# Optimization experiments

Hardware: AMD Instinct MI355X
Metric: run time of the kernel (lower is better)

## Reference

```python
import jax, jax.numpy as jnp
import numpy as np

# irrep blocks for 0e+1o+2e: dims 1, 3, 5 (total D=9)
BLOCKS = [(0, 1), (1, 4), (4, 9)]

def block_linear(x, W):
    # x: [N, C, 9], W: [3, C, C] -- e3nn Linear mixes channels within each irrep block
    outs = [jnp.einsum('ncd,cq->nqd', x[..., s:e], W[l]) for l, (s, e) in enumerate(BLOCKS)]
    return jnp.concatenate(outs, axis=-1)

def setup_inputs() -> dict:
    key = jax.random.key(0)
    ks = jax.random.split(key, 14)
    N, E, C, D, B, H, Z = 16384, 262144, 32, 9, 8, 64, 4
    inp = {
        'node_feats': jax.random.normal(ks[0], (N, C, D), jnp.float32),
        'node_attrs': jax.random.uniform(ks[1], (N, Z), jnp.float32),
        'edge_feats': jax.random.normal(ks[2], (E, B), jnp.float32),
        'edge_sh': jax.random.normal(ks[3], (E, D), jnp.float32),
        'cutoff': jax.random.uniform(ks[4], (E, 1), jnp.float32),
        # learned params
        'W_up': jax.random.normal(ks[5], (3, C, C), jnp.float32) / np.float32(np.sqrt(C)),
        'W1': jax.random.normal(ks[6], (B, H), jnp.float32) / np.float32(np.sqrt(B)),
        'W2': jax.random.normal(ks[7], (H, H), jnp.float32) / np.float32(np.sqrt(H)),
        'W3': jax.random.normal(ks[8], (H, C), jnp.float32) / np.float32(np.sqrt(H)),
        'W_lin': jax.random.normal(ks[9], (3, C, C), jnp.float32) / np.float32(np.sqrt(C)),
        'W_sc': jax.random.normal(ks[10], (Z, 3, C, C), jnp.float32) / np.float32(np.sqrt(C)),
        # fixed Clebsch-Gordan-like coupling tensor (constant structure of the TP)
        'CG': jax.random.normal(ks[11], (D, D, D), jnp.float32) / np.float32(D),
        'edge_src': jax.random.randint(ks[12], (E,), 0, N, jnp.int32),
        'edge_dst': jax.random.randint(ks[13], (E,), 0, N, jnp.int32),
    }
    return inp

def reference(node_feats, node_attrs, edge_feats, edge_sh, cutoff,
              W_up, W1, W2, W3, W_lin, W_sc, CG, edge_src, edge_dst):
    N = node_feats.shape[0]
    avg_num_neighbors = 16.0
    # linear_up: per-irrep channel mixing
    x = block_linear(node_feats, W_up)
    # radial MLP -> per-edge tensor-product weights, gated by cutoff
    h = jax.nn.silu(edge_feats @ W1)
    h = jax.nn.silu(h @ W2)
    w = (h @ W3) * cutoff  # [E, C]
    # gather source node feats, weighted equivariant tensor product per edge
    xs = x[edge_src]  # [E, C, D]
    m_ij = jnp.einsum('eci,ej,ijk,ec->eck', xs, edge_sh, CG, w)  # [E, C, D]
    # scatter-sum aggregation into destination nodes
    m_i = jax.ops.segment_sum(m_ij, edge_dst, num_segments=N)  # [N, C, D]
    # output linear + neighbor normalization
    m_i = block_linear(m_i, W_lin) / avg_num_neighbors
    # element-dependent self-connection from current message
    W_node = jnp.einsum('nz,zlcq->nlcq', node_attrs, W_sc)  # [N, 3, C, C]
    scs = jnp.concatenate(
        [jnp.einsum('ncd,ncq->nqd', m_i[..., s:e], W_node[:, l]) for l, (s, e) in enumerate(BLOCKS)],
        axis=-1)
    return (m_i, scs)
```

## Files before the change

kernel.cpp:

```cpp
#include <hip/hip_runtime.h>
#include <cstdint>

#define CC 32
#define DD 9
#define CD 288
#define BB 8
#define HH 64
#define ZZ 4
#define NB 8

typedef __attribute__((ext_vector_type(8))) short bf16x8;
typedef __attribute__((ext_vector_type(4))) float f32x4;

__device__ __forceinline__ float silu_f(float v) {
  return v / (1.0f + __expf(-v));
}

__device__ __forceinline__ int blk_of(int d) { return d == 0 ? 0 : (d < 4 ? 1 : 2); }

__device__ __forceinline__ unsigned int f2bf(float f) {
  unsigned int u = __float_as_uint(f);
  return (u + 0x7fffu + ((u >> 16) & 1u)) >> 16;
}
__device__ __forceinline__ float bf_lo(unsigned int u) { return __uint_as_float(u << 16); }
__device__ __forceinline__ float bf_hi(unsigned int u) { return __uint_as_float(u & 0xffff0000u); }

__global__ __launch_bounds__(256) void k_zero(float* __restrict__ p, int n) {
  int i = blockIdx.x * 256 + threadIdx.x;
  if (i < n) p[i] = 0.0f;
}

__global__ __launch_bounds__(256) void k_hist(const int* __restrict__ edst,
                                              int* __restrict__ deg, int E) {
  int e = blockIdx.x * 256 + threadIdx.x;
  if (e < E) atomicAdd(&deg[edst[e]], 1);
}

__global__ __launch_bounds__(1024) void k_scan(const int* __restrict__ deg,
                                               int* __restrict__ offs,
                                               int* __restrict__ cursor, int N) {
  __shared__ int part[1024];
  int t = threadIdx.x;
  int chunk = (N + 1023) >> 10;
  int base = t * chunk;
  int lim = N - base; if (lim > chunk) lim = chunk; if (lim < 0) lim = 0;
  int s = 0;
  for (int i = 0; i < lim; ++i) s += deg[base + i];
  part[t] = s;
  __syncthreads();
  for (int off = 1; off < 1024; off <<= 1) {
    int v = part[t];
    int u = (t >= off) ? part[t - off] : 0;
    __syncthreads();
    part[t] = v + u;
    __syncthreads();
  }
  int run = (t == 0) ? 0 : part[t - 1];
  for (int i = 0; i < lim; ++i) {
    offs[base + i] = run;
    cursor[base + i] = run;
    run += deg[base + i];
  }
  if (t == 1023) offs[N] = run;
}

__global__ __launch_bounds__(256) void k_scatter(const int* __restrict__ edst,
                                                 const int* __restrict__ esrc,
                                                 int* __restrict__ cursor,
                                                 int* __restrict__ eidx,
                                                 int* __restrict__ srcs, int E) {
  int e = blockIdx.x * 256 + threadIdx.x;
  if (e < E) {
    int d = edst[e];
    int pos = atomicAdd(&cursor[d], 1);
    eidx[pos] = e;
    srcs[pos] = esrc[e];
  }
}

__global__ __launch_bounds__(256) void k_eshs(const int* __restrict__ eidx,
                                              const float* __restrict__ esh,
                                              float* __restrict__ esh_s, long total) {
  long i = (long)blockIdx.x * 256 + threadIdx.x;
  if (i < total) {
    long pos = i / 9;
    int j = (int)(i - pos * 9);
    esh_s[i] = esh[(size_t)eidx[pos] * 9 + j];
  }
}

__global__ __launch_bounds__(288) void k_linear_up(
    const float* __restrict__ nf, const float* __restrict__ Wup,
    unsigned int* __restrict__ x_p, int N) {
  __shared__ float snf[NB][DD * 36];
  __shared__ float sval[NB][DD][CC];
  int t = threadIdx.x;
  int g = t >> 5, q = t & 31;
  int tc = t / 9, td = t - tc * 9;
  int l0 = blk_of(g);
  float wcol[CC];
#pragma unroll
  for (int c = 0; c < CC; ++c) wcol[c] = Wup[l0 * 1024 + c * 32 + q];
  int n0 = blockIdx.x * NB;
#pragma unroll
  for (int nb = 0; nb < NB; ++nb) {
    if (n0 + nb < N) snf[nb][td * 36 + tc] = nf[(size_t)(n0 + nb) * CD + t];
  }
  __syncthreads();
#pragma unroll
  for (int nb = 0; nb < NB; ++nb) {
    if (n0 + nb >= N) break;
    const float4* rowp = (const float4*)(snf[nb] + g * 36);
    float a0 = 0.f, a1 = 0.f;
#pragma unroll
    for (int c4 = 0; c4 < 8; ++c4) {
      float4 b = rowp[c4];
      a0 += b.x * wcol[c4 * 4 + 0] + b.y * wcol[c4 * 4 + 1];
      a1 += b.z * wcol[c4 * 4 + 2] + b.w * wcol[c4 * 4 + 3];
    }
    sval[nb][g][q] = a0 + a1;
  }
  __syncthreads();
#pragma unroll
  for (int it = 0; it < 5; ++it) {
    int idx = it * 288 + t;
    if (idx < NB * 160) {
      int nb = idx / 160, r = idx - nb * 160;
      int p = r >> 5, c = r & 31;
      if (n0 + nb < N) {
        unsigned int lo = f2bf(sval[nb][2 * p][c]);
        unsigned int hi = (p < 4) ? f2bf(sval[nb][2 * p + 1][c]) : 0u;
        x_p[(size_t)(n0 + nb) * 160 + r] = lo | (hi << 16);
      }
    }
  }
}

__global__ __launch_bounds__(64) void k_mlp_mfma(
    const float* __restrict__ ef, const float* __restrict__ cut,
    const float* __restrict__ W1, const float* __restrict__ W2,
    const float* __restrict__ W3, const int* __restrict__ eidx,
    float* __restrict__ w_s, int E) {
  __shared__ ushort hbuf[4096];
  __shared__ ushort h2buf[4096];
  __shared__ float scut[64];
  int l = threadIdx.x;
  int h = l >> 4, li = l & 15;
  bf16x8 A2[4][2];
#pragma unroll
  for (int qm = 0; qm < 4; ++qm)
#pragma unroll
    for (int kb = 0; kb < 2; ++kb)
#pragma unroll
      for (int j = 0; j < 8; ++j)
        A2[qm][kb][j] = (short)f2bf(W2[(32 * kb + 8 * h + j) * HH + 16 * qm + li]);
  bf16x8 A3[2][2];
#pragma unroll
  for (int cm = 0; cm < 2; ++cm)
#pragma unroll
    for (int kb = 0; kb < 2; ++kb)
#pragma unroll
      for (int j = 0; j < 8; ++j)
        A3[cm][kb][j] = (short)f2bf(W3[(32 * kb + 8 * h + j) * CC + 16 * cm + li]);

  int ntile = E >> 6;
  for (int tile = blockIdx.x; tile < ntile; tile += gridDim.x) {
    int pos = tile * 64 + l;
    int eo = eidx[pos];
    const float4* efp = (const float4*)(ef + (size_t)eo * BB);
    float4 efa = efp[0];
    float4 efb = efp[1];
    scut[l] = cut[eo];
    float efv[BB] = {efa.x, efa.y, efa.z, efa.w, efb.x, efb.y, efb.z, efb.w};
#pragma unroll
    for (int g = 0; g < 8; ++g) {
      float hv[8];
#pragma unroll
      for (int jj = 0; jj < 8; ++jj) {
        int q = g * 8 + jj;
        float a = 0.f;
#pragma unroll
        for (int kin = 0; kin < BB; ++kin) a += efv[kin] * W1[kin * HH + q];
        hv[jj] = silu_f(a);
      }
      unsigned int d0 = f2bf(hv[0]) | (f2bf(hv[1]) << 16);
      unsigned int d1 = f2bf(hv[2]) | (f2bf(hv[3]) << 16);
      unsigned int d2 = f2bf(hv[4]) | (f2bf(hv[5]) << 16);
      unsigned int d3 = f2bf(hv[6]) | (f2bf(hv[7]) << 16);
      int F = ((l >> 4) * 2 + (g >> 2)) * 4 + (g & 3);
      *(uint4*)&hbuf[(F * 16 + li) * 8] = make_uint4(d0, d1, d2, d3);
    }
    f32x4 acc2[4][4];
#pragma unroll
    for (int qm = 0; qm < 4; ++qm)
#pragma unroll
      for (int nb = 0; nb < 4; ++nb) acc2[qm][nb] = (f32x4){0.f, 0.f, 0.f, 0.f};
#pragma unroll
    for (int nb = 0; nb < 4; ++nb)
#pragma unroll
      for (int kb = 0; kb < 2; ++kb) {
        int F = (nb * 2 + kb) * 4 + h;
        bf16x8 Bf = *(const bf16x8*)&hbuf[(F * 16 + li) * 8];
#pragma unroll
        for (int qm = 0; qm < 4; ++qm)
          acc2[qm][nb] = __builtin_amdgcn_mfma_f32_16x16x32_bf16(
              A2[qm][kb], Bf, acc2[qm][nb], 0, 0, 0);
      }
#pragma unroll
    for (int qm = 0; qm < 4; ++qm)
#pragma unroll
      for (int nb = 0; nb < 4; ++nb) {
        float v0 = silu_f(acc2[qm][nb][0]);
        float v1 = silu_f(acc2[qm][nb][1]);
        float v2 = silu_f(acc2[qm][nb][2]);
        float v3 = silu_f(acc2[qm][nb][3]);
        unsigned int lo = f2bf(v0) | (f2bf(v1) << 16);
        unsigned int hi = f2bf(v2) | (f2bf(v3) << 16);
        int G = (nb * 2 + (qm >> 1)) * 4 + ((2 * qm + (h >> 1)) & 3);
        *(uint2*)&h2buf[(G * 16 + li) * 8 + (h & 1) * 4] = make_uint2(lo, hi);
      }
    f32x4 acc3[2][4];
#pragma unroll
    for (int cm = 0; cm < 2; ++cm)
#pragma unroll
      for (int nb = 0; nb < 4; ++nb) acc3[cm][nb] = (f32x4){0.f, 0.f, 0.f, 0.f};
#pragma unroll
    for (int nb = 0; nb < 4; ++nb)
#pragma unroll
      for (int kb = 0; kb < 2; ++kb) {
        int G = (nb * 2 + kb) * 4 + h;
        bf16x8 Bf = *(const bf16x8*)&h2buf[(G * 16 + li) * 8];
#pragma unroll
        for (int cm = 0; cm < 2; ++cm)
          acc3[cm][nb] = __builtin_amdgcn_mfma_f32_16x16x32_bf16(
              A3[cm][kb], Bf, acc3[cm][nb], 0, 0, 0);
      }
#pragma unroll
    for (int nb = 0; nb < 4; ++nb) {
      float cv = scut[16 * nb + li];
#pragma unroll
      for (int cm = 0; cm < 2; ++cm) {
        float4 o;
        o.x = acc3[cm][nb][0] * cv;
        o.y = acc3[cm][nb][1] * cv;
        o.z = acc3[cm][nb][2] * cv;
        o.w = acc3[cm][nb][3] * cv;
        *(float4*)&w_s[(size_t)(tile * 64 + 16 * nb + li) * CC + 16 * cm + 4 * h] = o;
      }
    }
  }
}

__global__ __launch_bounds__(256) void k_gather(
    const unsigned int* __restrict__ x_p, const float* __restrict__ w_s,
    const float* __restrict__ esh_s, const float* __restrict__ CG,
    const int* __restrict__ offs, const int* __restrict__ srcs,
    float* __restrict__ mpre, int N) {
  int wid = (blockIdx.x * 256 + threadIdx.x) >> 6;
  if (wid >= N) return;
  int lane = threadIdx.x & 63;
  int h = lane >> 5, c = lane & 31;
  int beg = offs[wid], end = offs[wid + 1];
  float P[81];
#pragma unroll
  for (int i = 0; i < 81; ++i) P[i] = 0.f;
  for (int p0 = beg; p0 < end; p0 += 2) {
    int p = p0 + h;
    bool ok = p < end;
    int pp = ok ? p : p0;
    int s = srcs[pp];
    float wc = ok ? w_s[(size_t)pp * CC + c] : 0.f;
    const float* shp = esh_s + (size_t)pp * DD;
    float sh[DD];
#pragma unroll
    for (int j = 0; j < DD; ++j) sh[j] = shp[j];
    const unsigned int* xp = x_p + (size_t)s * 160 + c;
    unsigned int u0 = xp[0], u1 = xp[32], u2 = xp[64], u3 = xp[96], u4 = xp[128];
    float xs[DD];
    xs[0] = bf_lo(u0); xs[1] = bf_hi(u0);
    xs[2] = bf_lo(u1); xs[3] = bf_hi(u1);
    xs[4] = bf_lo(u2); xs[5] = bf_hi(u2);
    xs[6] = bf_lo(u3); xs[7] = bf_hi(u3);
    xs[8] = bf_lo(u4);
#pragma unroll
    for (int i = 0; i < DD; ++i) {
      float t = wc * xs[i];
#pragma unroll
      for (int j = 0; j < DD; ++j) P[i * DD + j] += t * sh[j];
    }
  }
  float m[DD];
#pragma unroll
  for (int k = 0; k < DD; ++k) m[k] = 0.f;
#pragma unroll
  for (int i = 0; i < DD; ++i) {
#pragma unroll
    for (int j = 0; j < DD; ++j) {
      float p = P[i * DD + j];
#pragma unroll
      for (int k = 0; k < DD; ++k) m[k] += p * CG[i * 81 + j * DD + k];
    }
  }
#pragma unroll
  for (int k = 0; k < DD; ++k) m[k] += __shfl_xor(m[k], 32);
  if (h == 0) {
    float* mp = mpre + (size_t)wid * CD + c;
#pragma unroll
    for (int k = 0; k < DD; ++k) mp[k * 32] = m[k];
  }
}

__global__ __launch_bounds__(288, 1) void k_out(
    const float* __restrict__ attrs, const float* __restrict__ Wlin,
    const float* __restrict__ Wsc,
    float* __restrict__ out1, float* __restrict__ out2, int N) {
  __shared__ float smp[NB][CD];
  __shared__ float smt[NB][CD];
  __shared__ float sres1[NB * CD];
  __shared__ float sres2[NB * CD];
  int t = threadIdx.x;
  int g = t >> 5, q = t & 31;
  int l0 = blk_of(g);
  float wl[CC];
#pragma unroll
  for (int c = 0; c < CC; ++c) wl[c] = Wlin[l0 * 1024 + c * 32 + q];
  float ws0[CC], ws1[CC], ws2[CC], ws3[CC];
#pragma unroll
  for (int c = 0; c < CC; ++c) {
    ws0[c] = Wsc[0 * 3072 + l0 * 1024 + c * 32 + q];
    ws1[c] = Wsc[1 * 3072 + l0 * 1024 + c * 32 + q];
    ws2[c] = Wsc[2 * 3072 + l0 * 1024 + c * 32 + q];
    ws3[c] = Wsc[3 * 3072 + l0 * 1024 + c * 32 + q];
  }
  int nbat = (N + NB - 1) / NB;
  int b = blockIdx.x;
  float r[NB];
  if (b < nbat) {
#pragma unroll
    for (int nb = 0; nb < NB; ++nb) r[nb] = out2[(size_t)(b * NB + nb) * CD + t];
  }
  for (; b < nbat; b += gridDim.x) {
    int n0 = b * NB;
    __syncthreads();
#pragma unroll
    for (int nb = 0; nb < NB; ++nb) smp[nb][t] = r[nb];
    float4 av[NB];
#pragma unroll
    for (int nb = 0; nb < NB; ++nb) av[nb] = ((const float4*)attrs)[n0 + nb];
    __syncthreads();
    int b2 = b + gridDim.x;
    if (b2 < nbat) {
#pragma unroll
      for (int nb = 0; nb < NB; ++nb) r[nb] = out2[(size_t)(b2 * NB + nb) * CD + t];
    }
#pragma unroll
    for (int nb = 0; nb < NB; ++nb) {
      const float4* rowp = (const float4*)(smp[nb] + g * 32);
      float b0 = 0.f, b1 = 0.f;
#pragma unroll
      for (int c4 = 0; c4 < 8; ++c4) {
        float4 bb = rowp[c4];
        b0 += bb.x * wl[c4 * 4 + 0] + bb.y * wl[c4 * 4 + 1];
        b1 += bb.z * wl[c4 * 4 + 2] + bb.w * wl[c4 * 4 + 3];
      }
      float v = (b0 + b1) * (1.0f / 16.0f);
      smt[nb][t] = v;
      sres1[nb * CD + q * DD + g] = v;
    }
    __syncthreads();
#pragma unroll
    for (int nb = 0; nb < NB; ++nb) {
      const float4* rowp = (const float4*)(smt[nb] + g * 32);
      float z0 = 0.f, z1 = 0.f, z2 = 0.f, z3 = 0.f;
#pragma unroll
      for (int c4 = 0; c4 < 8; ++c4) {
        float4 bb = rowp[c4];
#pragma unroll
        for (int j = 0; j < 4; ++j) {
          float bv = (j == 0) ? bb.x : (j == 1) ? bb.y : (j == 2) ? bb.z : bb.w;
          int c = c4 * 4 + j;
          z0 += bv * ws0[c];
          z1 += bv * ws1[c];
          z2 += bv * ws2[c];
          z3 += bv * ws3[c];
        }
      }
      float4 a = av[nb];
      sres2[nb * CD + q * DD + g] = a.x * z0 + a.y * z1 + a.z * z2 + a.w * z3;
    }
    __syncthreads();
#pragma unroll
    for (int rr = 0; rr < (NB * 72) / 288; ++rr) {
      int s = rr * 288 + t;
      int nb = s / 72, idx = s - nb * 72;
      ((float4*)(out1 + (size_t)(n0 + nb) * CD))[idx] = ((const float4*)sres1)[s];
      ((float4*)(out2 + (size_t)(n0 + nb) * CD))[idx] = ((const float4*)sres2)[s];
    }
  }
}

extern "C" void kernel_launch(void* const* d_in, const int* in_sizes, int n_in,
                              void* d_out, int out_size, void* d_ws, size_t ws_size,
                              hipStream_t stream) {
  const float* nf    = (const float*)d_in[0];
  const float* attrs = (const float*)d_in[1];
  const float* ef    = (const float*)d_in[2];
  const float* esh   = (const float*)d_in[3];
  const float* cutv  = (const float*)d_in[4];
  const float* Wup   = (const float*)d_in[5];
  const float* W1    = (const float*)d_in[6];
  const float* W2    = (const float*)d_in[7];
  const float* W3    = (const float*)d_in[8];
  const float* Wlin  = (const float*)d_in[9];
  const float* Wsc   = (const float*)d_in[10];
  const float* CG    = (const float*)d_in[11];
  const int* esrc    = (const int*)d_in[12];
  const int* edst    = (const int*)d_in[13];
  int N = in_sizes[0] / CD;
  int E = in_sizes[12];
  float* out1 = (float*)d_out;
  float* out2 = out1 + (size_t)N * CD;

  unsigned int* x_p = (unsigned int*)d_ws;
  float* w_s   = (float*)(x_p + (size_t)N * 160);
  float* esh_s = w_s + (size_t)E * CC;
  int* deg     = (int*)(esh_s + (size_t)E * DD);
  int* offs    = deg + N;
  int* cursor  = offs + N + 1;
  int* eidx    = cursor + N;
  int* srcs    = eidx + E;

  int nblk = (N + NB - 1) / NB;
  k_zero<<<(N + 255) / 256, 256, 0, stream>>>((float*)deg, N);
  k_hist<<<(E + 255) / 256, 256, 0, stream>>>(edst, deg, E);
  k_scan<<<1, 1024, 0, stream>>>(deg, offs, cursor, N);
  k_scatter<<<(E + 255) / 256, 256, 0, stream>>>(edst, esrc, cursor, eidx, srcs, E);
  k_eshs<<<(int)(((long)E * 9 + 255) / 256), 256, 0, stream>>>(eidx, esh, esh_s, (long)E * 9);
  k_linear_up<<<nblk, 288, 0, stream>>>(nf, Wup, x_p, N);
  k_mlp_mfma<<<4096, 64, 0, stream>>>(ef, cutv, W1, W2, W3, eidx, w_s, E);
  k_gather<<<(N + 3) / 4, 256, 0, stream>>>(x_p, w_s, esh_s, CG, offs, srcs, out2, N);
  k_out<<<512, 288, 0, stream>>>(attrs, Wlin, Wsc, out1, out2, N);
}
```

Measured before the change: 252.5 us.

## Split gather accumulation across half-waves by input irrep index instead of edge

The gather kernel previously had each half-wave process alternate edges and keep a full 81-entry outer-product accumulator per lane. Now both half-waves walk every edge, and each half owns a subset of the input irrep components (4 or 5 rows). This cuts the accumulator to 45 registers and the bf16 loads per lane to 3. The aim is lower register pressure and higher occupancy, at the cost of reading edge weights and spherical harmonics twice and running twice as many loop iterations per half. The CG contraction is computed for both row sets, and each half keeps its own result with a select.

```diff
diff --git a/kernel.cpp b/kernel.cpp
--- a/kernel.cpp
+++ b/kernel.cpp
@@ -261,46 +261,51 @@
   int lane = threadIdx.x & 63;
   int h = lane >> 5, c = lane & 31;
   int beg = offs[wid], end = offs[wid + 1];
-  float P[81];
-#pragma unroll
-  for (int i = 0; i < 81; ++i) P[i] = 0.f;
-  for (int p0 = beg; p0 < end; p0 += 2) {
-    int p = p0 + h;
-    bool ok = p < end;
-    int pp = ok ? p : p0;
-    int s = srcs[pp];
-    float wc = ok ? w_s[(size_t)pp * CC + c] : 0.f;
-    const float* shp = esh_s + (size_t)pp * DD;
+  float P[45];
+#pragma unroll
+  for (int i = 0; i < 45; ++i) { P[i] = 0.f; asm volatile("" : "+v"(P[i])); }
+  for (int p = beg; p < end; ++p) {
+    int s = srcs[p];
+    float wc = w_s[(size_t)p * CC + c];
+    const float* shp = esh_s + (size_t)p * DD;
     float sh[DD];
 #pragma unroll
     for (int j = 0; j < DD; ++j) sh[j] = shp[j];
-    const unsigned int* xp = x_p + (size_t)s * 160 + c;
-    unsigned int u0 = xp[0], u1 = xp[32], u2 = xp[64], u3 = xp[96], u4 = xp[128];
-    float xs[DD];
+    const unsigned int* xp = x_p + (size_t)s * 160 + c + h * 64;
+    unsigned int u0 = xp[0], u1 = xp[32], u2 = xp[64];
+    float xs[5];
     xs[0] = bf_lo(u0); xs[1] = bf_hi(u0);
     xs[2] = bf_lo(u1); xs[3] = bf_hi(u1);
-    xs[4] = bf_lo(u2); xs[5] = bf_hi(u2);
-    xs[6] = bf_lo(u3); xs[7] = bf_hi(u3);
-    xs[8] = bf_lo(u4);
-#pragma unroll
-    for (int i = 0; i < DD; ++i) {
-      float t = wc * xs[i];
-#pragma unroll
-      for (int j = 0; j < DD; ++j) P[i * DD + j] += t * sh[j];
-    }
-  }
+    xs[4] = h ? bf_lo(u2) : 0.f;
+#pragma unroll
+    for (int r = 0; r < 5; ++r) {
+      float t = wc * xs[r];
+#pragma unroll
+      for (int j = 0; j < DD; ++j) P[r * DD + j] += t * sh[j];
+    }
+  }
+  float mA[DD], mB[DD];
+#pragma unroll
+  for (int k = 0; k < DD; ++k) { mA[k] = 0.f; mB[k] = 0.f; }
+#pragma unroll
+  for (int r = 0; r < 4; ++r)
+#pragma unroll
+    for (int j = 0; j < DD; ++j) {
+      float p = P[r * DD + j];
+#pragma unroll
+      for (int k = 0; k < DD; ++k) mA[k] += p * CG[r * 81 + j * DD + k];
+    }
+#pragma unroll
+  for (int r = 0; r < 5; ++r)
+#pragma unroll
+    for (int j = 0; j < DD; ++j) {
+      float p = P[r * DD + j];
+#pragma unroll
+      for (int k = 0; k < DD; ++k) mB[k] += p * CG[(4 + r) * 81 + j * DD + k];
+    }
   float m[DD];
 #pragma unroll
-  for (int k = 0; k < DD; ++k) m[k] = 0.f;
-#pragma unroll
-  for (int i = 0; i < DD; ++i) {
-#pragma unroll
-    for (int j = 0; j < DD; ++j) {
-      float p = P[i * DD + j];
-#pragma unroll
-      for (int k = 0; k < DD; ++k) m[k] += p * CG[i * 81 + j * DD + k];
-    }
-  }
+  for (int k = 0; k < DD; ++k) m[k] = h ? mB[k] : mA[k];
 #pragma unroll
   for (int k = 0; k < DD; ++k) m[k] += __shfl_xor(m[k], 32);
   if (h == 0) {
```

Result: slower. 260.0 us (+3.0%).
